# Performance work log

Hardware: AMD Instinct MI355X
Metric: run time of the kernel (lower is better)

## Reference

```python
import jax, jax.numpy as jnp
import numpy as np

DIM = 1024
HEADS = 16
DIM_HEADS = DIM // HEADS  # 64
DIM_HIDDEN = DIM_HEADS * HEADS


def setup_inputs() -> dict:
    key = jax.random.key(0)
    k1, k2, k3, k4, k5 = jax.random.split(key, 5)
    b, t = 2, 2048
    x = jax.random.normal(k1, (b, t, DIM), dtype=jnp.float32)
    # torch nn.Linear weights are [out_features, in_features]
    s = DIM ** -0.5
    W_q = jax.random.normal(k2, (DIM_HIDDEN, DIM), dtype=jnp.float32) * s
    W_kv = jax.random.normal(k3, (2 * DIM_HIDDEN, DIM), dtype=jnp.float32) * s
    W_out = jax.random.normal(k4, (DIM, DIM_HIDDEN), dtype=jnp.float32) * s
    b_out = jax.random.normal(k5, (DIM,), dtype=jnp.float32) * 0.01
    return {"x": x, "W_q": W_q, "W_kv": W_kv, "W_out": W_out, "b_out": b_out}


def reference(x, W_q, W_kv, W_out, b_out):
    b, t, d = x.shape
    h, e = HEADS, DIM_HEADS
    # projections (Linear: x @ W.T)
    q = jnp.einsum('btd,fd->btf', x, W_q)
    kv = jnp.einsum('btd,fd->btf', x, W_kv)
    k, v = jnp.split(kv, 2, axis=-1)
    # split heads -> (b, h, t, e)
    split = lambda z: z.reshape(b, t, h, e).transpose(0, 2, 1, 3)
    q, k, v = split(q), split(k), split(v)
    # scaled dot-product attention; original uses exp/sum/div softmax
    scores = jnp.einsum('bhqe,bhke->bhqk', q, k) * (e ** -0.5)
    attn = jax.nn.softmax(scores, axis=-1)
    out = jnp.einsum('bhqk,bhke->bhqe', attn, v)
    out = out.transpose(0, 2, 1, 3).reshape(b, t, h * e)
    return jnp.einsum('btf,df->btd', out, W_out) + b_out
```

## Files before the change

kernel.cpp:

```cpp
#include <hip/hip_runtime.h>
#include <hip/hip_bf16.h>

#define BB   2
#define TT   2048
#define DD   1024
#define HH   16
#define EE   64
#define BT   4096

typedef __attribute__((ext_vector_type(8))) short bf16x8;
typedef __attribute__((ext_vector_type(4))) float floatx4;
typedef __attribute__((ext_vector_type(16))) float floatx16;

__device__ __forceinline__ unsigned short f2bf(float f) {
  unsigned int x = __float_as_uint(f);
  x += 0x7fffu + ((x >> 16) & 1u);
  return (unsigned short)(x >> 16);
}
__device__ __forceinline__ unsigned int pack2u(float a, float b) {
  union { __hip_bfloat162 h; unsigned int u; } r;
  r.h = __float22bfloat162_rn(make_float2(a, b));
  return r.u;
}
__device__ __forceinline__ uint4 pack8(const float4& a, const float4& b) {
  union { uint4 u; __hip_bfloat162 h[4]; } r;
  r.h[0] = __float22bfloat162_rn(make_float2(a.x, a.y));
  r.h[1] = __float22bfloat162_rn(make_float2(a.z, a.w));
  r.h[2] = __float22bfloat162_rn(make_float2(b.x, b.y));
  r.h[3] = __float22bfloat162_rn(make_float2(b.z, b.w));
  return r.u;
}
__device__ __forceinline__ void ld16(unsigned short* lds, const unsigned short* g) {
  __builtin_amdgcn_global_load_lds(
      (const __attribute__((address_space(1))) unsigned int*)g,
      (__attribute__((address_space(3))) unsigned int*)lds, 16, 0, 0);
}

#define GX   524288
#define GWQ  131072
#define GWKV 262144
#define GWO  131072

__global__ __launch_bounds__(256) void convert_kernel(
    const float* __restrict__ X,  const float* __restrict__ Wq,
    const float* __restrict__ Wkv, const float* __restrict__ Wout,
    unsigned short* __restrict__ Xb, unsigned short* __restrict__ Wb,
    unsigned short* __restrict__ Wob) {
  int g = blockIdx.x * 256 + threadIdx.x;
  const float* src; unsigned short* dst; int gi;
  if (g < GX)                        { src = X;    dst = Xb;  gi = g; }
  else if ((g -= GX) < GWQ)          { src = Wq;   dst = Wb;  gi = g; }
  else if ((g -= GWQ) < GWKV)        { src = Wkv;  dst = Wb + (size_t)GWQ * 8; gi = g; }
  else                               { src = Wout; dst = Wob; gi = g - GWKV; }
  const float4* s4 = reinterpret_cast<const float4*>(src) + (size_t)gi * 2;
  float4 a = s4[0], b = s4[1];
  reinterpret_cast<uint4*>(dst)[gi] = pack8(a, b);
}

__global__ __launch_bounds__(256) void gemm_qkv_mfma(
    const unsigned short* __restrict__ Xb,
    const unsigned short* __restrict__ Wb,
    unsigned short* __restrict__ Qh,
    unsigned short* __restrict__ Kh,
    unsigned short* __restrict__ Vt) {
  __shared__ __align__(16) unsigned short smem[128 * 136];
  unsigned short* As = smem;
  unsigned short* Bs = smem + 128 * 64;
  const int tid  = threadIdx.x;
  const int lane = tid & 63, w = tid >> 6;
  const int wm = w >> 1, wn = w & 1;
  const int q = lane >> 4, c = lane & 15;
  const int bm0 = blockIdx.y * 128;
  const int bn0 = blockIdx.x * 128;
  const unsigned short* Ag = Xb + (size_t)bm0 * DD;
  const unsigned short* Bg = Wb + (size_t)bn0 * DD;

  floatx4 acc[4][4];
#pragma unroll
  for (int i = 0; i < 4; ++i)
#pragma unroll
    for (int j = 0; j < 4; ++j) acc[i][j] = (floatx4){0.f, 0.f, 0.f, 0.f};

  int prow[4], pch[4];
#pragma unroll
  for (int t = 0; t < 4; ++t) {
    int s = (w * 4 + t) * 64 + lane;
    prow[t] = s >> 3;
    pch[t]  = (s & 7) ^ (prow[t] & 7);
  }
  int aoff[4][2], boff[4][2];
#pragma unroll
  for (int i = 0; i < 4; ++i)
#pragma unroll
    for (int h = 0; h < 2; ++h) {
      aoff[i][h] = (wm * 64 + i * 16 + c) * 64 + (((q + h * 4) ^ (c & 7)) << 3);
      boff[i][h] = (wn * 64 + i * 16 + c) * 64 + (((q + h * 4) ^ (c & 7)) << 3);
    }

  for (int kk = 0; kk < DD; kk += 64) {
    __syncthreads();
#pragma unroll
    for (int t = 0; t < 4; ++t) {
      int i = w * 4 + t;
      ld16(&As[i * 512], &Ag[(size_t)prow[t] * DD + kk + pch[t] * 8]);
      ld16(&Bs[i * 512], &Bg[(size_t)prow[t] * DD + kk + pch[t] * 8]);
    }
    __syncthreads();
    bf16x8 af[4][2], bfr[4][2];
#pragma unroll
    for (int i = 0; i < 4; ++i)
#pragma unroll
      for (int h = 0; h < 2; ++h) {
        af[i][h]  = *reinterpret_cast<const bf16x8*>(&As[aoff[i][h]]);
        bfr[i][h] = *reinterpret_cast<const bf16x8*>(&Bs[boff[i][h]]);
      }
#pragma unroll
    for (int i = 0; i < 4; ++i)
#pragma unroll
      for (int j = 0; j < 4; ++j) {
        acc[i][j] = __builtin_amdgcn_mfma_f32_16x16x32_bf16(af[i][0], bfr[j][0], acc[i][j], 0, 0, 0);
        acc[i][j] = __builtin_amdgcn_mfma_f32_16x16x32_bf16(af[i][1], bfr[j][1], acc[i][j], 0, 0, 0);
      }
  }

  const int region = bn0 >> 10;
  if (region < 2) {
    const float scl = (region == 0) ? 0.18033688011112042f : 1.0f;
    __syncthreads();
    unsigned short* tb = smem;
#pragma unroll
    for (int i = 0; i < 4; ++i) {
#pragma unroll
      for (int j = 0; j < 4; ++j) {
        int n  = wn * 64 + j * 16 + c;
        int m0 = wm * 64 + i * 16 + q * 4;
#pragma unroll
        for (int reg = 0; reg < 4; ++reg)
          tb[(m0 + reg) * 136 + n] = f2bf(acc[i][j][reg] * scl);
      }
    }
    __syncthreads();
    unsigned short* dst = (region == 0) ? Qh : Kh;
    const int b   = bm0 >> 11;
    const int t0  = bm0 & 2047;
    const int nb0 = bn0 & 1023;
    const int oct = tid & 15;
    const int nb  = nb0 + oct * 8;
    const int h   = nb >> 6, e = nb & 63;
#pragma unroll
    for (int it = 0; it < 8; ++it) {
      int tr = it * 16 + (tid >> 4);
      uint4 vv = *reinterpret_cast<const uint4*>(&tb[tr * 136 + oct * 8]);
      *reinterpret_cast<uint4*>(
          &dst[((size_t)((b * HH + h) * TT + t0 + tr)) * EE + e]) = vv;
    }
  } else {
    __syncthreads();
    unsigned short* tb = smem;
#pragma unroll
    for (int i = 0; i < 4; ++i) {
#pragma unroll
      for (int j = 0; j < 4; ++j) {
        int nl = wn * 64 + j * 16 + c;
        int ml = wm * 64 + i * 16 + q * 4;
        ushort4 pk;
        pk.x = f2bf(acc[i][j][0]);
        pk.y = f2bf(acc[i][j][1]);
        pk.z = f2bf(acc[i][j][2]);
        pk.w = f2bf(acc[i][j][3]);
        *reinterpret_cast<ushort4*>(&tb[nl * 136 + ml]) = pk;
      }
    }
    __syncthreads();
    const int b  = bm0 >> 11;
    const int t0 = bm0 & 2047;
    const int nb0 = bn0 & 1023;
    const int lr = tid & 15;
#pragma unroll
    for (int it = 0; it < 8; ++it) {
      int nl = it * 16 + (tid >> 4);
      int nb = nb0 + nl;
      int h = nb >> 6, e = nb & 63;
      uint4 vv = *reinterpret_cast<const uint4*>(&tb[nl * 136 + lr * 8]);
      *reinterpret_cast<uint4*>(
          &Vt[((size_t)(b * HH + h) * EE + e) * TT + t0 + lr * 8]) = vv;
    }
  }
}

#define NKT 32
#define VST 68

#define ATILE(P, PREF, VMC)                                                    \
  do {                                                                         \
    if (PREF) {                                                                \
      _Pragma("unroll")                                                        \
      for (int t = 0; t < 4; ++t) {                                            \
        vreg[t] = *reinterpret_cast<const uint4*>(vpre[t]);                    \
        vpre[t] += 64;                                                         \
      }                                                                        \
      _Pragma("unroll")                                                        \
      for (int t = 0; t < 4; ++t) {                                            \
        ld16(&Kbuf[((P) ^ 1) * 4096 + (t * 2 + w) * 512], kpre[t]);            \
        kpre[t] += 4096;                                                       \
      }                                                                        \
    }                                                                          \
    asm volatile("s_waitcnt vmcnt(" VMC ")" ::: "memory");                     \
    asm volatile("s_barrier" ::: "memory");                                    \
    bf16x8 kf[2][4];                                                           \
    _Pragma("unroll")                                                          \
    for (int nt = 0; nt < 2; ++nt)                                             \
      _Pragma("unroll")                                                        \
      for (int kc = 0; kc < 4; ++kc)                                           \
        kf[nt][kc] = *reinterpret_cast<const bf16x8*>(                         \
            &Kbuf[(P) * 4096 + koff[nt][kc]]);                                 \
    floatx16 sacc[2];                                                          \
    _Pragma("unroll")                                                          \
    for (int nt = 0; nt < 2; ++nt) {                                           \
      sacc[nt] = __builtin_amdgcn_mfma_f32_32x32x16_bf16(kf[nt][0], qf[0], zf, 0, 0, 0); \
      _Pragma("unroll")                                                        \
      for (int kc = 1; kc < 4; ++kc)                                           \
        sacc[nt] = __builtin_amdgcn_mfma_f32_32x32x16_bf16(kf[nt][kc], qf[kc], sacc[nt], 0, 0, 0); \
    }                                                                          \
    unsigned int pp[2][8];                                                     \
    _Pragma("unroll")                                                          \
    for (int nt = 0; nt < 2; ++nt)                                             \
      _Pragma("unroll")                                                        \
      for (int r = 0; r < 8; ++r) {                                            \
        float e0 = __builtin_amdgcn_exp2f(sacc[nt][2 * r]);                    \
        float e1 = __builtin_amdgcn_exp2f(sacc[nt][2 * r + 1]);                \
        pp[nt][r] = pack2u(e0, e1);                                            \
      }                                                                        \
    _Pragma("unroll")                                                          \
    for (int nt = 0; nt < 2; ++nt)                                             \
      _Pragma("unroll")                                                        \
      for (int kcp = 0; kcp < 2; ++kcp) {                                      \
        union { unsigned int u[4]; bf16x8 v; } pf;                             \
        pf.u[0] = pp[nt][4 * kcp + 0]; pf.u[1] = pp[nt][4 * kcp + 1];          \
        pf.u[2] = pp[nt][4 * kcp + 2]; pf.u[3] = pp[nt][4 * kcp + 3];          \
        lacc = __builtin_amdgcn_mfma_f32_32x32x16_bf16(pf.v, onesf.v, lacc, 0, 0, 0); \
        _Pragma("unroll")                                                      \
        for (int eh = 0; eh < 2; ++eh) {                                       \
          const int cc = nt * 4 + 2 * kcp;                                     \
          uint2 v0 = *reinterpret_cast<const uint2*>(                          \
              &Vbuf[(P) * 4352 + voff[eh][cc]]);                               \
          uint2 v1 = *reinterpret_cast<const uint2*>(                          \
              &Vbuf[(P) * 4352 + voff[eh][cc + 1]]);                           \
          union { unsigned int u[4]; bf16x8 v; } vf;                           \
          vf.u[0] = v0.x; vf.u[1] = v0.y; vf.u[2] = v1.x; vf.u[3] = v1.y;      \
          o_acc[eh] = __builtin_amdgcn_mfma_f32_32x32x16_bf16(pf.v, vf.v, o_acc[eh], 0, 0, 0); \
        }                                                                      \
      }                                                                        \
    if (PREF) {                                                                \
      asm volatile("s_waitcnt vmcnt(4)" ::: "memory");                         \
      _Pragma("unroll")                                                        \
      for (int t = 0; t < 4; ++t) {                                            \
        unsigned short* vd = &Vbuf[((P) ^ 1) * 4352 + vwoff[t]];               \
        *reinterpret_cast<uint2*>(vd)     = make_uint2(vreg[t].x, vreg[t].y);  \
        *reinterpret_cast<uint2*>(vd + 4) = make_uint2(vreg[t].z, vreg[t].w);  \
      }                                                                        \
      asm volatile("s_waitcnt lgkmcnt(0)" ::: "memory");                       \
    }                                                                          \
    asm volatile("s_barrier" ::: "memory");                                    \
  } while (0)

__global__ __launch_bounds__(128) void attn_kernel(
    const unsigned short* __restrict__ Qh,
    const unsigned short* __restrict__ Kh,
    const unsigned short* __restrict__ Vtg,
    unsigned short* __restrict__ Aw) {
  __shared__ __align__(16) unsigned short smem[16896];

  const int tid  = threadIdx.x;
  const int lane = tid & 63;
  const int w    = tid >> 6;
  const int n31  = lane & 31;
  const int g    = lane >> 5;

  const int flat = blockIdx.y * 32 + blockIdx.x;
  const int idx  = flat >> 3;
  const int bh   = (flat & 7) * 4 + (idx >> 5);
  const int qt   = idx & 31;
  const size_t base = (size_t)bh * TT * EE;
  const unsigned short* Qp = Qh + base + (size_t)(qt * 64 + w * 32) * EE;
  const unsigned short* Kp = Kh + base;
  const unsigned short* Vp = Vtg + base;

  unsigned short* Kbuf = smem;
  unsigned short* Vbuf = smem + 8192;

  union { unsigned int u[4]; bf16x8 v; } onesf;
  onesf.u[0] = 0x3F803F80u; onesf.u[1] = 0x3F803F80u;
  onesf.u[2] = 0x3F803F80u; onesf.u[3] = 0x3F803F80u;

  const floatx16 zf = (floatx16)(0.0f);

  bf16x8 qf[4];
#pragma unroll
  for (int kc = 0; kc < 4; ++kc)
    qf[kc] = *reinterpret_cast<const bf16x8*>(
        &Qp[(size_t)n31 * EE + kc * 16 + g * 8]);

  int srow[4], sch[4], voct[4], vwoff[4];
#pragma unroll
  for (int t = 0; t < 4; ++t) {
    int s = (t * 2 + w) * 64 + lane;
    srow[t] = s >> 3;
    sch[t]  = (s & 7) ^ (srow[t] & 7);
    voct[t] = s & 7;
    vwoff[t] = srow[t] * VST + voct[t] * 8;
  }

  int koff[2][4];
#pragma unroll
  for (int nt = 0; nt < 2; ++nt) {
    const int krow = nt * 32 + n31;
#pragma unroll
    for (int kc = 0; kc < 4; ++kc)
      koff[nt][kc] = krow * 64 + (((kc * 2 + g) ^ (krow & 7)) << 3);
  }
  int voff[2][8];
#pragma unroll
  for (int eh = 0; eh < 2; ++eh) {
    const int vrow = eh * 32 + n31;
#pragma unroll
    for (int cc = 0; cc < 8; ++cc)
      voff[eh][cc] = vrow * VST + cc * 8 + g * 4;
  }

  const unsigned short* kpre[4];
  const unsigned short* vpre[4];
#pragma unroll
  for (int t = 0; t < 4; ++t) {
    kpre[t] = Kp + (size_t)(64 + srow[t]) * EE + sch[t] * 8;
    vpre[t] = Vp + (size_t)srow[t] * TT + 64 + voct[t] * 8;
  }

  floatx16 o_acc[2];
  o_acc[0] = (floatx16)(0.0f);
  o_acc[1] = (floatx16)(0.0f);
  floatx16 lacc = (floatx16)(0.0f);

  uint4 vreg[4];

#pragma unroll
  for (int t = 0; t < 4; ++t)
    vreg[t] = *reinterpret_cast<const uint4*>(
        Vp + (size_t)srow[t] * TT + voct[t] * 8);
#pragma unroll
  for (int t = 0; t < 4; ++t)
    ld16(&Kbuf[(t * 2 + w) * 512], Kp + (size_t)srow[t] * EE + sch[t] * 8);
  asm volatile("s_waitcnt vmcnt(4)" ::: "memory");
#pragma unroll
  for (int t = 0; t < 4; ++t) {
    unsigned short* vd = &Vbuf[vwoff[t]];
    *reinterpret_cast<uint2*>(vd)     = make_uint2(vreg[t].x, vreg[t].y);
    *reinterpret_cast<uint2*>(vd + 4) = make_uint2(vreg[t].z, vreg[t].w);
  }
  asm volatile("s_waitcnt lgkmcnt(0)" ::: "memory");

  for (int kt2 = 0; kt2 < 15; ++kt2) {
    ATILE(0, true, "8");
    ATILE(1, true, "8");
  }
  ATILE(0, true, "8");
  ATILE(1, false, "0");

  const int b = bh >> 4, h = bh & 15;
#pragma unroll
  for (int eh = 0; eh < 2; ++eh)
#pragma unroll
    for (int reg = 0; reg < 16; ++reg) {
      int qrl = (reg & 3) + 8 * (reg >> 2) + 4 * g;
      int t = qt * 64 + w * 32 + qrl;
      Aw[((size_t)(b * TT + t)) * DD + h * EE + eh * 32 + n31] =
          f2bf(o_acc[eh][reg] * (1.0f / lacc[reg]));
    }
}

__global__ __launch_bounds__(256) void gemm_out_mfma(
    const unsigned short* __restrict__ A,
    const unsigned short* __restrict__ Wob,
    const float* __restrict__ bias,
    float* __restrict__ out) {
  __shared__ __align__(16) unsigned short As[128 * 64];
  __shared__ __align__(16) unsigned short Bs[64 * 64];
  const int tid  = threadIdx.x;
  const int lane = tid & 63, w = tid >> 6;
  const int wm = w >> 1, wn = w & 1;
  const int q = lane >> 4, c = lane & 15;
  const int bm0 = blockIdx.y * 128;
  const int bn0 = blockIdx.x * 64;
  const unsigned short* Ag = A + (size_t)bm0 * DD;
  const unsigned short* Bg = Wob + (size_t)bn0 * DD;

  floatx4 acc[4][2];
#pragma unroll
  for (int i = 0; i < 4; ++i)
#pragma unroll
    for (int j = 0; j < 2; ++j) acc[i][j] = (floatx4){0.f, 0.f, 0.f, 0.f};

  int parow[4], pach[4];
#pragma unroll
  for (int t = 0; t < 4; ++t) {
    int s = (w * 4 + t) * 64 + lane;
    parow[t] = s >> 3;
    pach[t]  = (s & 7) ^ (parow[t] & 7);
  }
  int pbrow[2], pbch[2];
#pragma unroll
  for (int t = 0; t < 2; ++t) {
    int s = (w * 2 + t) * 64 + lane;
    pbrow[t] = s >> 3;
    pbch[t]  = (s & 7) ^ (pbrow[t] & 7);
  }

  for (int kk = 0; kk < DD; kk += 64) {
    __syncthreads();
#pragma unroll
    for (int t = 0; t < 4; ++t)
      ld16(&As[(w * 4 + t) * 512], &Ag[(size_t)parow[t] * DD + kk + pach[t] * 8]);
#pragma unroll
    for (int t = 0; t < 2; ++t)
      ld16(&Bs[(w * 2 + t) * 512], &Bg[(size_t)pbrow[t] * DD + kk + pbch[t] * 8]);
    __syncthreads();
    bf16x8 af[4][2], bfr[2][2];
#pragma unroll
    for (int h = 0; h < 2; ++h) {
      int ksw = ((q + h * 4) ^ (c & 7)) << 3;
#pragma unroll
      for (int i = 0; i < 4; ++i)
        af[i][h] = *reinterpret_cast<const bf16x8*>(&As[(wm * 64 + i * 16 + c) * 64 + ksw]);
#pragma unroll
      for (int j = 0; j < 2; ++j)
        bfr[j][h] = *reinterpret_cast<const bf16x8*>(&Bs[(wn * 32 + j * 16 + c) * 64 + ksw]);
    }
#pragma unroll
    for (int i = 0; i < 4; ++i)
#pragma unroll
      for (int j = 0; j < 2; ++j) {
        acc[i][j] = __builtin_amdgcn_mfma_f32_16x16x32_bf16(af[i][0], bfr[j][0], acc[i][j], 0, 0, 0);
        acc[i][j] = __builtin_amdgcn_mfma_f32_16x16x32_bf16(af[i][1], bfr[j][1], acc[i][j], 0, 0, 0);
      }
  }

#pragma unroll
  for (int i = 0; i < 4; ++i) {
#pragma unroll
    for (int j = 0; j < 2; ++j) {
      int n = bn0 + wn * 32 + j * 16 + c;
      float bv = bias[n];
#pragma unroll
      for (int reg = 0; reg < 4; ++reg) {
        int m = bm0 + wm * 64 + i * 16 + q * 4 + reg;
        out[(size_t)m * DD + n] = acc[i][j][reg] + bv;
      }
    }
  }
}

extern "C" void kernel_launch(void* const* d_in, const int* in_sizes, int n_in,
                              void* d_out, int out_size, void* d_ws, size_t ws_size,
                              hipStream_t stream) {
  const float* X    = (const float*)d_in[0];
  const float* Wq   = (const float*)d_in[1];
  const float* Wkv  = (const float*)d_in[2];
  const float* Wout = (const float*)d_in[3];
  const float* bout = (const float*)d_in[4];
  float* out = (float*)d_out;

  unsigned short* Qh  = (unsigned short*)d_ws;
  unsigned short* Kh  = Qh + (size_t)BT * DD;
  unsigned short* Vt  = Kh + (size_t)BT * DD;
  unsigned short* Aw  = Vt + (size_t)BT * DD;
  unsigned short* Xb  = Aw;
  unsigned short* Wb  = Aw + (size_t)BT * DD;
  unsigned short* Wob = Wb + (size_t)3 * 1024 * DD;

  convert_kernel<<<dim3(4096), 256, 0, stream>>>(X, Wq, Wkv, Wout, Xb, Wb, Wob);
  gemm_qkv_mfma<<<dim3(24, 32), 256, 0, stream>>>(Xb, Wb, Qh, Kh, Vt);
  attn_kernel<<<dim3(32, 32), 128, 0, stream>>>(Qh, Kh, Vt, Aw);
  gemm_out_mfma<<<dim3(16, 32), 256, 0, stream>>>(Aw, Wob, bout, out);
}
```

Before: 190.2 us.

## Double-buffer LDS in output-projection GEMM with async prefetch of next K tile

Converts the output projection GEMM from a single-buffered load-sync-compute loop to a double-buffered pipeline. The next K tile is prefetched into the alternate LDS buffer while MFMAs run on the current one, and explicit vmcnt waits plus barriers replace the two __syncthreads per iteration. This targets the global-load latency exposed in each K step, at the cost of twice the LDS footprint and reliance on hand-counted vmcnt values.

```diff
diff --git a/kernel.cpp b/kernel.cpp
--- a/kernel.cpp
+++ b/kernel.cpp
@@ -378,13 +378,52 @@
     }
 }
 
+#define GTILE(P, PREF, VMC)                                                    \
+  do {                                                                         \
+    if (PREF) {                                                                \
+      _Pragma("unroll")                                                        \
+      for (int t = 0; t < 4; ++t) {                                            \
+        ld16(&As[((P) ^ 1) * 8192 + (w * 4 + t) * 512], apre[t]);              \
+        apre[t] += 64;                                                         \
+      }                                                                        \
+      _Pragma("unroll")                                                        \
+      for (int t = 0; t < 2; ++t) {                                            \
+        ld16(&Bs[((P) ^ 1) * 4096 + (w * 2 + t) * 512], bpre[t]);              \
+        bpre[t] += 64;                                                         \
+      }                                                                        \
+    }                                                                          \
+    asm volatile("s_waitcnt vmcnt(" VMC ")" ::: "memory");                     \
+    asm volatile("s_barrier" ::: "memory");                                    \
+    bf16x8 af[4][2], bfr[2][2];                                                \
+    _Pragma("unroll")                                                          \
+    for (int h = 0; h < 2; ++h) {                                              \
+      const int ksw = ((q + h * 4) ^ (c & 7)) << 3;                            \
+      _Pragma("unroll")                                                        \
+      for (int i = 0; i < 4; ++i)                                              \
+        af[i][h] = *reinterpret_cast<const bf16x8*>(                           \
+            &As[(P) * 8192 + (wm * 64 + i * 16 + c) * 64 + ksw]);              \
+      _Pragma("unroll")                                                        \
+      for (int j = 0; j < 2; ++j)                                              \
+        bfr[j][h] = *reinterpret_cast<const bf16x8*>(                          \
+            &Bs[(P) * 4096 + (wn * 32 + j * 16 + c) * 64 + ksw]);              \
+    }                                                                          \
+    _Pragma("unroll")                                                          \
+    for (int i = 0; i < 4; ++i)                                                \
+      _Pragma("unroll")                                                        \
+      for (int j = 0; j < 2; ++j) {                                            \
+        acc[i][j] = __builtin_amdgcn_mfma_f32_16x16x32_bf16(af[i][0], bfr[j][0], acc[i][j], 0, 0, 0); \
+        acc[i][j] = __builtin_amdgcn_mfma_f32_16x16x32_bf16(af[i][1], bfr[j][1], acc[i][j], 0, 0, 0); \
+      }                                                                        \
+    asm volatile("s_barrier" ::: "memory");                                    \
+  } while (0)
+
 __global__ __launch_bounds__(256) void gemm_out_mfma(
     const unsigned short* __restrict__ A,
     const unsigned short* __restrict__ Wob,
     const float* __restrict__ bias,
     float* __restrict__ out) {
-  __shared__ __align__(16) unsigned short As[128 * 64];
-  __shared__ __align__(16) unsigned short Bs[64 * 64];
+  __shared__ __align__(16) unsigned short As[2 * 128 * 64];
+  __shared__ __align__(16) unsigned short Bs[2 * 64 * 64];
   const int tid  = threadIdx.x;
   const int lane = tid & 63, w = tid >> 6;
   const int wm = w >> 1, wn = w & 1;
@@ -415,34 +454,28 @@
     pbch[t]  = (s & 7) ^ (pbrow[t] & 7);
   }
 
-  for (int kk = 0; kk < DD; kk += 64) {
-    __syncthreads();
-#pragma unroll
-    for (int t = 0; t < 4; ++t)
-      ld16(&As[(w * 4 + t) * 512], &Ag[(size_t)parow[t] * DD + kk + pach[t] * 8]);
-#pragma unroll
-    for (int t = 0; t < 2; ++t)
-      ld16(&Bs[(w * 2 + t) * 512], &Bg[(size_t)pbrow[t] * DD + kk + pbch[t] * 8]);
-    __syncthreads();
-    bf16x8 af[4][2], bfr[2][2];
-#pragma unroll
-    for (int h = 0; h < 2; ++h) {
-      int ksw = ((q + h * 4) ^ (c & 7)) << 3;
-#pragma unroll
-      for (int i = 0; i < 4; ++i)
-        af[i][h] = *reinterpret_cast<const bf16x8*>(&As[(wm * 64 + i * 16 + c) * 64 + ksw]);
-#pragma unroll
-      for (int j = 0; j < 2; ++j)
-        bfr[j][h] = *reinterpret_cast<const bf16x8*>(&Bs[(wn * 32 + j * 16 + c) * 64 + ksw]);
-    }
-#pragma unroll
-    for (int i = 0; i < 4; ++i)
-#pragma unroll
-      for (int j = 0; j < 2; ++j) {
-        acc[i][j] = __builtin_amdgcn_mfma_f32_16x16x32_bf16(af[i][0], bfr[j][0], acc[i][j], 0, 0, 0);
-        acc[i][j] = __builtin_amdgcn_mfma_f32_16x16x32_bf16(af[i][1], bfr[j][1], acc[i][j], 0, 0, 0);
-      }
-  }
+  const unsigned short* apre[4];
+  const unsigned short* bpre[2];
+#pragma unroll
+  for (int t = 0; t < 4; ++t)
+    apre[t] = Ag + (size_t)parow[t] * DD + 64 + pach[t] * 8;
+#pragma unroll
+  for (int t = 0; t < 2; ++t)
+    bpre[t] = Bg + (size_t)pbrow[t] * DD + 64 + pbch[t] * 8;
+
+#pragma unroll
+  for (int t = 0; t < 4; ++t)
+    ld16(&As[(w * 4 + t) * 512], Ag + (size_t)parow[t] * DD + pach[t] * 8);
+#pragma unroll
+  for (int t = 0; t < 2; ++t)
+    ld16(&Bs[(w * 2 + t) * 512], Bg + (size_t)pbrow[t] * DD + pbch[t] * 8);
+
+  for (int kt2 = 0; kt2 < 7; ++kt2) {
+    GTILE(0, true, "6");
+    GTILE(1, true, "6");
+  }
+  GTILE(0, true, "6");
+  GTILE(1, false, "0");
 
 #pragma unroll
   for (int i = 0; i < 4; ++i) {
```

Result: slower. 194.3 us (+2.1%).
